# Kernel optimization log

Hardware: AMD Instinct MI355X
Metric: run time of the kernel (lower is better)

Reference implementation:

```python
import jax, jax.numpy as jnp
import numpy as np

B, T, H, W = 512, 8, 28, 28
VTH, VRESET = 1.0, 0.0
ALPHA = 2.0  # spikingjelly ATan surrogate default alpha


@jax.custom_vjp
def heaviside_atan(x):
    # forward: binary spike; backward: ATan surrogate gradient
    return (x >= 0).astype(x.dtype)

def _ha_fwd(x):
    return (x >= 0).astype(x.dtype), x

def _ha_bwd(x, g):
    return (g * (ALPHA / 2.0) / (1.0 + (jnp.pi / 2.0 * ALPHA * x) ** 2),)

heaviside_atan.defvjp(_ha_fwd, _ha_bwd)


def conv3x3(x, w):
    return jax.lax.conv_general_dilated(
        x, w, (1, 1), 'SAME', dimension_numbers=('NCHW', 'OIHW', 'NCHW'))


def maxpool2(x):
    return jax.lax.reduce_window(x, -jnp.inf, jax.lax.max,
                                 (1, 1, 2, 2), (1, 1, 2, 2), 'VALID')


def one_spike_if(v, fired, x):
    # OneSpikeIFNode: integrate, fire at most once (fired mask), hard reset
    v = v + x
    spike = heaviside_atan(v - VTH) * (1.0 - fired)
    v = v * (1.0 - spike) + VRESET * spike
    fired = jnp.maximum(fired, jax.lax.stop_gradient(spike))
    return v, fired, spike


def if_node(v, x):
    # readout IFNode: integrate, fire, hard reset (v_threshold finite: latency mode, no warmup)
    v = v + x
    spike = heaviside_atan(v - VTH)
    v = v * (1.0 - spike) + VRESET * spike
    return v, spike


def setup_inputs() -> dict:
    key = jax.random.key(0)
    k = jax.random.split(key, 5)
    x = jax.random.uniform(k[0], (B, 1, H, W), jnp.float32)
    # weight scale (default_T / T) == 1 since T == 8 == default_T
    w_sconv = jax.random.normal(k[1], (16, 1, 3, 3), jnp.float32) * (2.0 / 3.0)
    w_conv = jax.random.normal(k[2], (16, 16, 3, 3), jnp.float32) * 0.12
    w_fc1 = jax.random.normal(k[3], (100, 16 * 14 * 14), jnp.float32) * 0.02
    w_fc2 = jax.random.normal(k[4], (10, 100), jnp.float32) * 0.15
    return {"x": x, "w_sconv": w_sconv, "w_conv": w_conv, "w_fc1": w_fc1, "w_fc2": w_fc2}


def reference(x, w_sconv, w_conv, w_fc1, w_fc2):
    xs = conv3x3(x, w_sconv)  # static conv computed once, reused every timestep
    z = jnp.zeros_like(xs)                       # [B,16,28,28]
    zp = jnp.zeros((B, 16, 14, 14), xs.dtype)    # pool fired-window mask
    zf = jnp.zeros((B, 100), xs.dtype)
    zo = jnp.zeros((B, 10), xs.dtype)
    state0 = (z, z, z, z, zp, zf, zf, zo)

    def step(state, _):
        v1, f1, v2, f2, pf, vfc, ffc, vout = state
        v1, f1, s1 = one_spike_if(v1, f1, xs)
        c = conv3x3(s1, w_conv)
        v2, f2, s2 = one_spike_if(v2, f2, c)
        # FirstSpikePool2d: max-pool spikes, each window passes only its first spike
        pooled = maxpool2(s2) * (1.0 - pf)
        pf = jnp.maximum(pf, jax.lax.stop_gradient(pooled))
        h = pooled.reshape(B, -1) @ w_fc1.T      # [B,100]
        vfc, ffc, s3 = one_spike_if(vfc, ffc, h)
        o = s3 @ w_fc2.T                          # [B,10]
        vout, s4 = if_node(vout, o)
        fr = jnp.stack([s1.mean(), s2.mean(), s3.mean(), s4.mean()])
        return (v1, f1, v2, f2, pf, vfc, ffc, vout), (s4, vout, fr)

    _, (s4_t, vout_t, fr_t) = jax.lax.scan(step, state0, None, length=T)
    counter_t = jnp.cumsum(s4_t, axis=0)                        # [T,B,10]
    latency_score = heaviside_atan(counter_t - 0.5).sum(axis=0)  # ATan_binary surrogate
    reg_loss = fr_t.max(axis=0).sum()
    return latency_score / T, reg_loss
```

## Files before the change

### kernel.cpp

```cpp
#include <hip/hip_runtime.h>

#define TB 1024
#define NIMG 512
#define HW 28
#define NPIX 784
#define TT 8
#define NFC 100
#define NOUT 10
#define MAGIC 0x5C5C5C5Cu

#define WT_FLOATS 313600
#define GLB_ADD(p, v) __hip_atomic_fetch_add((p), (v), __ATOMIC_RELAXED, __HIP_MEMORY_SCOPE_AGENT)

typedef float f4 __attribute__((ext_vector_type(4)));

__global__ __launch_bounds__(TB, 8)
void snn_main(const float* __restrict__ xg, const float* __restrict__ w_sconv,
              const float* __restrict__ w_conv, const float* __restrict__ w_fc1,
              const float* __restrict__ w_fc2, float* __restrict__ wT,
              float* __restrict__ out, unsigned int* __restrict__ ctrl)
{
    __shared__ float wc[2880];
    __shared__ unsigned char spanB[25600];
    __shared__ unsigned short rowOr[TT * HW];
    __shared__ unsigned char tqA[3136];
    __shared__ unsigned short slist[3136];
    __shared__ float xst[NPIX];
    __shared__ float wsc[144];
    __shared__ int bcnt[9], bofs[9], bput[8];
    __shared__ int hist[32];
    __shared__ int lastflag;

    unsigned short* mask_t = (unsigned short*)spanB;
    unsigned int* mask32 = (unsigned int*)spanB;
    unsigned int* t2n = (unsigned int*)(spanB + 12544);
    float* prefixLDS = (float*)spanB;

    unsigned int* tflags = ctrl;
    float* fr_g = (float*)(ctrl + 98);
    unsigned int* done2 = ctrl + 130;
    unsigned int* fr_ready = ctrl + 131;

    const int tid = threadIdx.x;
    const int b = blockIdx.x;

    if (b < 98) {
        const int c0 = b * 32;
        for (int idx = tid; idx < 3200; idx += TB) {
            int c = idx / 100, r = idx - 100 * c;
            wT[(c0 + c) * 100 + r] = w_fc1[r * 3136 + c0 + c];
        }
    }
    if (b == 0 && tid < 33) ctrl[98 + tid] = 0u;

    for (int i = tid; i < NPIX; i += TB) xst[i] = xg[b * NPIX + i];
    for (int i = tid; i < 144; i += TB) wsc[i] = w_sconv[i];
    for (int i = tid; i < 2304; i += TB) {
        int c = i & 15, r = i >> 4;
        wc[r * 20 + c] = w_conv[c * 144 + r];
    }
    for (int i = tid; i < 3136; i += TB) mask32[i] = 0u;
    if (tid < 32) hist[tid] = 0;
    if (tid < 9) bcnt[tid] = 0;
    if (b < 98) __threadfence();
    __syncthreads();
    if (b < 98 && tid == 0) {
        __hip_atomic_store(&tflags[b], MAGIC, __ATOMIC_RELEASE, __HIP_MEMORY_SCOPE_AGENT);
        if (b == 0)
            __hip_atomic_store(fr_ready, MAGIC, __ATOMIC_RELEASE, __HIP_MEMORY_SCOPE_AGENT);
    }

    unsigned int pca = 0, pcb = 0;
#pragma unroll 1
    for (int e = 0; e < 13; e++) {
        int g = e * TB + tid;
        if (g < 12544) {
            int ci = g & 15, pos = g >> 4;
            int yy = pos / HW, xx = pos % HW;
            float acc = 0.f;
#pragma unroll
            for (int ky = 0; ky < 3; ky++) {
                int ys = yy + ky - 1;
                if (ys < 0 || ys >= HW) continue;
#pragma unroll
                for (int kx = 0; kx < 3; kx++) {
                    int xsrc = xx + kx - 1;
                    if (xsrc < 0 || xsrc >= HW) continue;
                    acc = fmaf(wsc[ci * 9 + ky * 3 + kx], xst[ys * HW + xsrc], acc);
                }
            }
            int t1 = 8; float v = 0.f;
#pragma unroll
            for (int t = 0; t < TT; t++) {
                v += acc;
                if (t1 == 8 && v >= 1.0f) t1 = t;
            }
            if (t1 < 8) {
                int lin = t1 * NPIX + pos;
                atomicOr(&mask32[lin >> 1], (1u << ci) << ((lin & 1) * 16));
                if (t1 < 4) pca += 1u << (t1 * 8); else pcb += 1u << ((t1 - 4) * 8);
            }
        }
    }
#pragma unroll
    for (int t = 0; t < TT; t++) {
        unsigned int c = ((t < 4 ? (pca >> (t * 8)) : (pcb >> ((t - 4) * 8))) & 255u);
        if (c) atomicAdd(&hist[t], (int)c);
    }
    __syncthreads();

    for (int i = tid; i < TT * HW; i += TB) {
        const unsigned short* mr = mask_t + (i / HW) * NPIX + (i % HW) * HW;
        unsigned int o = 0;
#pragma unroll
        for (int x = 0; x < HW; x++) o |= mr[x];
        rowOr[i] = (unsigned short)o;
    }
    __syncthreads();

    unsigned int pc2a = 0, pc2b = 0;
    {
        int pos = tid;
        if (pos < NPIX) {
            int py = pos / HW, px = pos - py * HW;
            f4 vv0 = {0.f, 0.f, 0.f, 0.f}, vv1 = vv0, vv2 = vv0, vv3 = vv0;
            unsigned int done = 0;
            unsigned int t2lo = 0x88888888u, t2hi = 0x88888888u;
#pragma unroll 1
            for (int t = 0; t < TT; t++) {
                const unsigned short* ro = rowOr + t * HW;
                unsigned int un = ro[py];
                if (py > 0) un |= ro[py - 1];
                if (py < HW - 1) un |= ro[py + 1];
                if (!un) continue;
                const unsigned short* mt = mask_t + t * NPIX;
#pragma unroll
                for (int k = 0; k < 9; k++) {
                    int qy = py + k / 3 - 1, qx = px + k % 3 - 1;
                    if ((unsigned)qy >= HW || (unsigned)qx >= HW) continue;
                    unsigned int m = mt[qy * HW + qx];
                    while (m) {
                        int ci = __builtin_ctz(m); m &= m - 1;
                        const f4* wrow = (const f4*)&wc[(ci * 9 + k) * 20];
                        vv0 += wrow[0]; vv1 += wrow[1];
                        vv2 += wrow[2]; vv3 += wrow[3];
                    }
                }
                unsigned int fired = 0;
#pragma unroll
                for (int c = 0; c < 16; c++) {
                    float val = (c < 4) ? vv0[c & 3] : (c < 8) ? vv1[c & 3]
                              : (c < 12) ? vv2[c & 3] : vv3[c & 3];
                    fired |= (val >= 1.0f) ? (1u << c) : 0u;
                }
                unsigned int newf = fired & ~done;
                done |= newf;
                if (newf) {
                    int cnt = __builtin_popcount(newf);
                    if (t < 4) pc2a += (unsigned)cnt << (t * 8);
                    else       pc2b += (unsigned)cnt << ((t - 4) * 8);
                    while (newf) {
                        int c = __builtin_ctz(newf); newf &= newf - 1;
                        if (c < 8) t2lo = (t2lo & ~(15u << (4 * c))) | ((unsigned)t << (4 * c));
                        else       t2hi = (t2hi & ~(15u << (4 * (c - 8)))) | ((unsigned)t << (4 * (c - 8)));
                    }
                }
                if (done == 0xffffu) break;
            }
            t2n[pos * 2] = t2lo;
            t2n[pos * 2 + 1] = t2hi;
        }
    }
#pragma unroll
    for (int t = 0; t < TT; t++) {
        unsigned int c = ((t < 4 ? (pc2a >> (t * 8)) : (pc2b >> ((t - 4) * 8))) & 255u);
        if (c) atomicAdd(&hist[8 + t], (int)c);
    }
    __syncthreads();

    for (int u = tid; u < 3136; u += TB) {
        int c = u / 196, rem = u - c * 196;
        int wy = rem / 14, wx = rem - wy * 14;
        int p0 = wy * 56 + wx * 2;
        int wsel = c >> 3, sh = (c & 7) * 4;
        int m0 = (t2n[p0 * 2 + wsel] >> sh) & 15;
        int m1 = (t2n[(p0 + 1) * 2 + wsel] >> sh) & 15;
        int m2 = (t2n[(p0 + HW) * 2 + wsel] >> sh) & 15;
        int m3 = (t2n[(p0 + HW + 1) * 2 + wsel] >> sh) & 15;
        int tqv = min(min(m0, m1), min(m2, m3));
        tqA[u] = (unsigned char)tqv;
        if (tqv < 8) atomicAdd(&bcnt[tqv], 1);
    }
    __syncthreads();
    if (tid == 0) {
        int s = 0;
#pragma unroll
        for (int t = 0; t < TT; t++) { bofs[t] = s; s += bcnt[t]; }
        bofs[8] = s;
    }
    __syncthreads();
    if (tid < 8) bput[tid] = bofs[tid];
    __syncthreads();
    for (int u = tid; u < 3136; u += TB) {
        int tqv = tqA[u];
        if (tqv < 8) { int j = atomicAdd(&bput[tqv], 1); slist[j] = (unsigned short)u; }
    }

    if (tid < 98) {
        while (__hip_atomic_load(&tflags[tid], __ATOMIC_ACQUIRE,
                                 __HIP_MEMORY_SCOPE_AGENT) != MAGIC)
            __builtin_amdgcn_s_sleep(2);
    }
    __syncthreads();

    {
        const int lane = tid & 63;
        const int w = tid >> 7;
        const int sub = (tid >> 6) & 1;
        const int col = sub * 64 + lane;
        const bool act = col < NFC;
        const float* wA = wT + col;
        float acc0 = 0.f;
#pragma unroll 1
        for (int t = 0; t < TT; t++) {
            const int lo = bofs[t];
            const int n = bofs[t + 1] - lo;
            int j = w;
            for (; j + 24 < n; j += 32) {
                int u0 = (int)slist[lo + j] * 100;
                int u1 = (int)slist[lo + j + 8] * 100;
                int u2 = (int)slist[lo + j + 16] * 100;
                int u3 = (int)slist[lo + j + 24] * 100;
                if (act) {
                    float a0 = wA[u0], a1 = wA[u1], a2 = wA[u2], a3 = wA[u3];
                    acc0 += a0; acc0 += a1; acc0 += a2; acc0 += a3;
                }
            }
            for (; j < n; j += 8) {
                int u0 = (int)slist[lo + j] * 100;
                if (act) acc0 += wA[u0];
            }
            if (act) prefixLDS[(w * TT + t) * NFC + col] = acc0;
        }
    }
    __syncthreads();

    if (tid < NFC) {
        int t3 = 8;
#pragma unroll
        for (int t = 0; t < TT; t++) {
            float v = 0.f;
#pragma unroll
            for (int w = 0; w < 8; w++) v += prefixLDS[(w * TT + t) * NFC + tid];
            if (t3 == 8 && v >= 1.0f) t3 = t;
        }
        tqA[tid] = (unsigned char)t3;
        if (t3 < 8) atomicAdd(&hist[16 + t3], 1);
    }
    __syncthreads();

    if (tid < NOUT) {
        float acc8[TT] = {0.f, 0.f, 0.f, 0.f, 0.f, 0.f, 0.f, 0.f};
        for (int i = 0; i < NFC; i++) {
            float w = w_fc2[tid * NFC + i];
            int tv = tqA[i];
#pragma unroll
            for (int k = 0; k < TT; k++) acc8[k] += (tv == k) ? w : 0.f;
        }
        float vout = 0.f; int cnt = 0; float lat = 0.f;
#pragma unroll
        for (int t = 0; t < TT; t++) {
            vout += acc8[t];
            if (vout >= 1.0f) { vout = 0.f; cnt++; atomicAdd(&hist[24 + t], 1); }
            if (cnt >= 1) lat += 1.f;
        }
        out[b * NOUT + tid] = lat * 0.125f;
    }
    __syncthreads();

    if (tid == 0) {
        while (__hip_atomic_load(fr_ready, __ATOMIC_ACQUIRE,
                                 __HIP_MEMORY_SCOPE_AGENT) != MAGIC)
            __builtin_amdgcn_s_sleep(2);
    }
    __syncthreads();
    if (tid < 32) {
        int h = hist[tid];
        if (h) GLB_ADD(&fr_g[(tid & 7) * 4 + (tid >> 3)], (float)h);
    }
    __syncthreads();

    if (tid == 0) {
        unsigned int old = __hip_atomic_fetch_add(done2, 1u, __ATOMIC_ACQ_REL,
                                                  __HIP_MEMORY_SCOPE_AGENT);
        lastflag = (old == (unsigned)(NIMG - 1));
    }
    __syncthreads();
    if (lastflag && tid == 0) {
        const float inv0 = 1.f / 6422528.f;
        const float inv2 = 1.f / 51200.f;
        const float inv3 = 1.f / 5120.f;
        const float invs[4] = { inv0, inv0, inv2, inv3 };
        float reg = 0.f;
        for (int l = 0; l < 4; l++) {
            float mx = -INFINITY;
            for (int t = 0; t < TT; t++) {
                float v = __hip_atomic_load(&fr_g[t * 4 + l], __ATOMIC_RELAXED,
                                            __HIP_MEMORY_SCOPE_AGENT);
                mx = fmaxf(mx, v * invs[l]);
            }
            reg += mx;
        }
        out[NIMG * NOUT] = reg;
    }
}

extern "C" void kernel_launch(void* const* d_in, const int* in_sizes, int n_in,
                              void* d_out, int out_size, void* d_ws, size_t ws_size,
                              hipStream_t stream) {
    const float* x       = (const float*)d_in[0];
    const float* w_sconv = (const float*)d_in[1];
    const float* w_conv  = (const float*)d_in[2];
    const float* w_fc1   = (const float*)d_in[3];
    const float* w_fc2   = (const float*)d_in[4];
    float* out = (float*)d_out;

    float* wT          = (float*)d_ws;
    unsigned int* ctrl = (unsigned int*)(wT + WT_FLOATS);

    snn_main<<<NIMG, TB, 0, stream>>>(x, w_sconv, w_conv, w_fc1, w_fc2, wT,
                                      out, ctrl);
}
```

Baseline: 186.4 us.

## Use wave reductions for histograms, ballot-based bucketing, and wave-parallel fc2

Replaces per-thread LDS atomics for the spike-time histograms and bucket counts with packed-byte wave shuffle reductions, so one lane per wave issues the atomics. Builds the sparse spike list with ballot/popcount compaction, one atomic per wave per timestep. Remaps the conv2 pixel assignment to a permuted run order, unrolls the fc1 gather loop to 8 loads, and spreads the fc2 readout across 10 waves with shuffle reductions instead of 10 serial threads. This targets LDS atomic contention and serial tails, at the cost of more shuffle instructions and extra registers.

Measured after the change: 173.5 us. 1.07x faster.

```diff
diff --git a/kernel.cpp b/kernel.cpp
--- a/kernel.cpp
+++ b/kernel.cpp
@@ -13,6 +13,17 @@
 #define GLB_ADD(p, v) __hip_atomic_fetch_add((p), (v), __ATOMIC_RELAXED, __HIP_MEMORY_SCOPE_AGENT)
 
 typedef float f4 __attribute__((ext_vector_type(4)));
+
+__device__ __forceinline__ void wave_sum4(unsigned int& a, unsigned int& b,
+                                          unsigned int& c, unsigned int& d) {
+#pragma unroll
+    for (int s = 1; s < 64; s <<= 1) {
+        a += __shfl_xor(a, s);
+        b += __shfl_xor(b, s);
+        c += __shfl_xor(c, s);
+        d += __shfl_xor(d, s);
+    }
+}
 
 __global__ __launch_bounds__(TB, 8)
 void snn_main(const float* __restrict__ xg, const float* __restrict__ w_sconv,
@@ -43,6 +54,7 @@
 
     const int tid = threadIdx.x;
     const int b = blockIdx.x;
+    const int lane = tid & 63;
 
     if (b < 98) {
         const int c0 = b * 32;
@@ -102,10 +114,20 @@
             }
         }
     }
-#pragma unroll
-    for (int t = 0; t < TT; t++) {
-        unsigned int c = ((t < 4 ? (pca >> (t * 8)) : (pcb >> ((t - 4) * 8))) & 255u);
-        if (c) atomicAdd(&hist[t], (int)c);
+    {
+        unsigned int a_lo = pca & 0x00ff00ffu, a_hi = (pca >> 8) & 0x00ff00ffu;
+        unsigned int b_lo = pcb & 0x00ff00ffu, b_hi = (pcb >> 8) & 0x00ff00ffu;
+        wave_sum4(a_lo, a_hi, b_lo, b_hi);
+        if (lane == 0) {
+            if (a_lo & 0xffffu)  atomicAdd(&hist[0], (int)(a_lo & 0xffffu));
+            if (a_hi & 0xffffu)  atomicAdd(&hist[1], (int)(a_hi & 0xffffu));
+            if (a_lo >> 16)      atomicAdd(&hist[2], (int)(a_lo >> 16));
+            if (a_hi >> 16)      atomicAdd(&hist[3], (int)(a_hi >> 16));
+            if (b_lo & 0xffffu)  atomicAdd(&hist[4], (int)(b_lo & 0xffffu));
+            if (b_hi & 0xffffu)  atomicAdd(&hist[5], (int)(b_hi & 0xffffu));
+            if (b_lo >> 16)      atomicAdd(&hist[6], (int)(b_lo >> 16));
+            if (b_hi >> 16)      atomicAdd(&hist[7], (int)(b_hi >> 16));
+        }
     }
     __syncthreads();
 
@@ -120,8 +142,9 @@
 
     unsigned int pc2a = 0, pc2b = 0;
     {
-        int pos = tid;
-        if (pos < NPIX) {
+        int run = tid >> 4;
+        int pos = (run < 49) ? ((run * 18) % 49) * 16 + (tid & 15) : -1;
+        if (pos >= 0) {
             int py = pos / HW, px = pos - py * HW;
             f4 vv0 = {0.f, 0.f, 0.f, 0.f}, vv1 = vv0, vv2 = vv0, vv3 = vv0;
             unsigned int done = 0;
@@ -171,25 +194,54 @@
             t2n[pos * 2 + 1] = t2hi;
         }
     }
-#pragma unroll
-    for (int t = 0; t < TT; t++) {
-        unsigned int c = ((t < 4 ? (pc2a >> (t * 8)) : (pc2b >> ((t - 4) * 8))) & 255u);
-        if (c) atomicAdd(&hist[8 + t], (int)c);
-    }
-    __syncthreads();
-
-    for (int u = tid; u < 3136; u += TB) {
-        int c = u / 196, rem = u - c * 196;
-        int wy = rem / 14, wx = rem - wy * 14;
-        int p0 = wy * 56 + wx * 2;
-        int wsel = c >> 3, sh = (c & 7) * 4;
-        int m0 = (t2n[p0 * 2 + wsel] >> sh) & 15;
-        int m1 = (t2n[(p0 + 1) * 2 + wsel] >> sh) & 15;
-        int m2 = (t2n[(p0 + HW) * 2 + wsel] >> sh) & 15;
-        int m3 = (t2n[(p0 + HW + 1) * 2 + wsel] >> sh) & 15;
-        int tqv = min(min(m0, m1), min(m2, m3));
-        tqA[u] = (unsigned char)tqv;
-        if (tqv < 8) atomicAdd(&bcnt[tqv], 1);
+    {
+        unsigned int a_lo = pc2a & 0x00ff00ffu, a_hi = (pc2a >> 8) & 0x00ff00ffu;
+        unsigned int b_lo = pc2b & 0x00ff00ffu, b_hi = (pc2b >> 8) & 0x00ff00ffu;
+        wave_sum4(a_lo, a_hi, b_lo, b_hi);
+        if (lane == 0) {
+            if (a_lo & 0xffffu)  atomicAdd(&hist[8],  (int)(a_lo & 0xffffu));
+            if (a_hi & 0xffffu)  atomicAdd(&hist[9],  (int)(a_hi & 0xffffu));
+            if (a_lo >> 16)      atomicAdd(&hist[10], (int)(a_lo >> 16));
+            if (a_hi >> 16)      atomicAdd(&hist[11], (int)(a_hi >> 16));
+            if (b_lo & 0xffffu)  atomicAdd(&hist[12], (int)(b_lo & 0xffffu));
+            if (b_hi & 0xffffu)  atomicAdd(&hist[13], (int)(b_hi & 0xffffu));
+            if (b_lo >> 16)      atomicAdd(&hist[14], (int)(b_lo >> 16));
+            if (b_hi >> 16)      atomicAdd(&hist[15], (int)(b_hi >> 16));
+        }
+    }
+    __syncthreads();
+
+    {
+        unsigned int cpa = 0, cpb = 0;
+        for (int u = tid; u < 3136; u += TB) {
+            int c = u / 196, rem = u - c * 196;
+            int wy = rem / 14, wx = rem - wy * 14;
+            int p0 = wy * 56 + wx * 2;
+            int wsel = c >> 3, sh = (c & 7) * 4;
+            int m0 = (t2n[p0 * 2 + wsel] >> sh) & 15;
+            int m1 = (t2n[(p0 + 1) * 2 + wsel] >> sh) & 15;
+            int m2 = (t2n[(p0 + HW) * 2 + wsel] >> sh) & 15;
+            int m3 = (t2n[(p0 + HW + 1) * 2 + wsel] >> sh) & 15;
+            int tqv = min(min(m0, m1), min(m2, m3));
+            tqA[u] = (unsigned char)tqv;
+            if (tqv < 8) {
+                if (tqv < 4) cpa += 1u << (tqv * 8);
+                else         cpb += 1u << ((tqv - 4) * 8);
+            }
+        }
+        unsigned int a_lo = cpa & 0x00ff00ffu, a_hi = (cpa >> 8) & 0x00ff00ffu;
+        unsigned int b_lo = cpb & 0x00ff00ffu, b_hi = (cpb >> 8) & 0x00ff00ffu;
+        wave_sum4(a_lo, a_hi, b_lo, b_hi);
+        if (lane == 0) {
+            if (a_lo & 0xffffu)  atomicAdd(&bcnt[0], (int)(a_lo & 0xffffu));
+            if (a_hi & 0xffffu)  atomicAdd(&bcnt[1], (int)(a_hi & 0xffffu));
+            if (a_lo >> 16)      atomicAdd(&bcnt[2], (int)(a_lo >> 16));
+            if (a_hi >> 16)      atomicAdd(&bcnt[3], (int)(a_hi >> 16));
+            if (b_lo & 0xffffu)  atomicAdd(&bcnt[4], (int)(b_lo & 0xffffu));
+            if (b_hi & 0xffffu)  atomicAdd(&bcnt[5], (int)(b_hi & 0xffffu));
+            if (b_lo >> 16)      atomicAdd(&bcnt[6], (int)(b_lo >> 16));
+            if (b_hi >> 16)      atomicAdd(&bcnt[7], (int)(b_hi >> 16));
+        }
     }
     __syncthreads();
     if (tid == 0) {
@@ -201,9 +253,22 @@
     __syncthreads();
     if (tid < 8) bput[tid] = bofs[tid];
     __syncthreads();
-    for (int u = tid; u < 3136; u += TB) {
-        int tqv = tqA[u];
-        if (tqv < 8) { int j = atomicAdd(&bput[tqv], 1); slist[j] = (unsigned short)u; }
+    for (int base_u = 0; base_u < 3136; base_u += TB) {
+        int u = base_u + tid;
+        int tqv = (u < 3136) ? (int)tqA[u] : 8;
+#pragma unroll 1
+        for (int v = 0; v < TT; v++) {
+            unsigned long long m = __ballot(tqv == v);
+            if (!m) continue;
+            int lead = __ffsll((unsigned long long)m) - 1;
+            int bs = 0;
+            if (lane == lead) bs = atomicAdd(&bput[v], __popcll(m));
+            bs = __shfl(bs, lead);
+            if (tqv == v) {
+                int rank = __popcll(m & ((1ull << lane) - 1ull));
+                slist[bs + rank] = (unsigned short)u;
+            }
+        }
     }
 
     if (tid < 98) {
@@ -214,7 +279,6 @@
     __syncthreads();
 
     {
-        const int lane = tid & 63;
         const int w = tid >> 7;
         const int sub = (tid >> 6) & 1;
         const int col = sub * 64 + lane;
@@ -226,6 +290,22 @@
             const int lo = bofs[t];
             const int n = bofs[t + 1] - lo;
             int j = w;
+            for (; j + 56 < n; j += 64) {
+                int u0 = (int)slist[lo + j] * 100;
+                int u1 = (int)slist[lo + j + 8] * 100;
+                int u2 = (int)slist[lo + j + 16] * 100;
+                int u3 = (int)slist[lo + j + 24] * 100;
+                int u4 = (int)slist[lo + j + 32] * 100;
+                int u5 = (int)slist[lo + j + 40] * 100;
+                int u6 = (int)slist[lo + j + 48] * 100;
+                int u7 = (int)slist[lo + j + 56] * 100;
+                if (act) {
+                    float a0 = wA[u0], a1 = wA[u1], a2 = wA[u2], a3 = wA[u3];
+                    float a4 = wA[u4], a5 = wA[u5], a6 = wA[u6], a7 = wA[u7];
+                    acc0 += a0; acc0 += a1; acc0 += a2; acc0 += a3;
+                    acc0 += a4; acc0 += a5; acc0 += a6; acc0 += a7;
+                }
+            }
             for (; j + 24 < n; j += 32) {
                 int u0 = (int)slist[lo + j] * 100;
                 int u1 = (int)slist[lo + j + 8] * 100;
@@ -259,22 +339,36 @@
     }
     __syncthreads();
 
-    if (tid < NOUT) {
+    if (tid < 640) {
+        const int o = tid >> 6;
         float acc8[TT] = {0.f, 0.f, 0.f, 0.f, 0.f, 0.f, 0.f, 0.f};
-        for (int i = 0; i < NFC; i++) {
-            float w = w_fc2[tid * NFC + i];
-            int tv = tqA[i];
-#pragma unroll
-            for (int k = 0; k < TT; k++) acc8[k] += (tv == k) ? w : 0.f;
-        }
-        float vout = 0.f; int cnt = 0; float lat = 0.f;
-#pragma unroll
-        for (int t = 0; t < TT; t++) {
-            vout += acc8[t];
-            if (vout >= 1.0f) { vout = 0.f; cnt++; atomicAdd(&hist[24 + t], 1); }
-            if (cnt >= 1) lat += 1.f;
-        }
-        out[b * NOUT + tid] = lat * 0.125f;
+        {
+            float wv = w_fc2[o * NFC + lane];
+            int tv = tqA[lane];
+#pragma unroll
+            for (int k = 0; k < TT; k++) acc8[k] += (tv == k) ? wv : 0.f;
+        }
+        if (lane < 36) {
+            float wv = w_fc2[o * NFC + 64 + lane];
+            int tv = tqA[64 + lane];
+#pragma unroll
+            for (int k = 0; k < TT; k++) acc8[k] += (tv == k) ? wv : 0.f;
+        }
+#pragma unroll
+        for (int s = 1; s < 64; s <<= 1) {
+#pragma unroll
+            for (int k = 0; k < TT; k++) acc8[k] += __shfl_xor(acc8[k], s);
+        }
+        if (lane == 0) {
+            float vout = 0.f; int cnt = 0; float lat = 0.f;
+#pragma unroll
+            for (int t = 0; t < TT; t++) {
+                vout += acc8[t];
+                if (vout >= 1.0f) { vout = 0.f; cnt++; atomicAdd(&hist[24 + t], 1); }
+                if (cnt >= 1) lat += 1.f;
+            }
+            out[b * NOUT + o] = lat * 0.125f;
+        }
     }
     __syncthreads();
 
```
